# Optimization experiments

Hardware: AMD Instinct MI355X
Metric: run time of the kernel (lower is better)

Reference implementation:

```python
import jax, jax.numpy as jnp
import numpy as np
import math

B, L, DM, H, DK, DFF, E, FACTOR = 4, 2048, 512, 8, 64, 2048, 3, 5
U = min(FACTOR * math.ceil(math.log(L)), L)  # 40: ProbSparse sample/top-k count
SCALE = 1.0 / math.sqrt(DK)
EPS = 1e-5


def setup_inputs() -> dict:
    key = jax.random.key(0)
    ks = jax.random.split(key, 24)
    w = lambda k, s: jax.random.normal(k, s, jnp.float32) * 0.02
    inp = {
        "DNAs": jax.random.normal(ks[0], (B, L, 4), jnp.float32),
        "W_pre": w(ks[1], (4, DM)), "b_pre": jnp.zeros((DM,), jnp.float32),
        "Wq": w(ks[2], (E, DM, DM)), "bq": jnp.zeros((E, DM), jnp.float32),
        "Wk": w(ks[3], (E, DM, DM)), "bk": jnp.zeros((E, DM), jnp.float32),
        "Wv": w(ks[4], (E, DM, DM)), "bv": jnp.zeros((E, DM), jnp.float32),
        "Wo": w(ks[5], (E, DM, DM)), "bo": jnp.zeros((E, DM), jnp.float32),
        "ln1_g": jnp.ones((E, DM), jnp.float32), "ln1_b": jnp.zeros((E, DM), jnp.float32),
        "W1": w(ks[6], (E, DM, DFF)), "b1": jnp.zeros((E, DFF), jnp.float32),
        "W2": w(ks[7], (E, DFF, DM)), "b2": jnp.zeros((E, DM), jnp.float32),
        "ln2_g": jnp.ones((E, DM), jnp.float32), "ln2_b": jnp.zeros((E, DM), jnp.float32),
        "lnf_g": jnp.ones((DM,), jnp.float32), "lnf_b": jnp.zeros((DM,), jnp.float32),
        "W_out": w(ks[8], (DM, 3)), "b_out": jnp.zeros((3,), jnp.float32),
        "sample_idx": jax.random.randint(ks[9], (L, U), 0, L, dtype=jnp.int32),
    }
    return inp


def layer_norm(x, g, b):
    m = jnp.mean(x, axis=-1, keepdims=True)
    v = jnp.mean((x - m) ** 2, axis=-1, keepdims=True)
    return (x - m) / jnp.sqrt(v + EPS) * g + b


def prob_attention(q, k, v, idx):
    # q,k,v: (B,H,L,DK); idx: (L,U) sampled key positions per query
    Ks = k[:, :, idx, :]                                   # (B,H,L,U,DK)
    qk = jnp.einsum('bhld,bhlud->bhlu', q, Ks)             # sampled scores
    M = qk.max(axis=-1) - qk.mean(axis=-1)                 # sparsity measure (B,H,L)
    _, top = jax.lax.top_k(M, U)                           # top-U "active" queries (B,H,U)
    q_red = jnp.take_along_axis(q, top[..., None], axis=2) # (B,H,U,DK)
    scores = jnp.einsum('bhud,bhkd->bhuk', q_red, k) * SCALE
    attn = jax.nn.softmax(scores, axis=-1)
    upd = jnp.einsum('bhuk,bhkd->bhud', attn, v)           # (B,H,U,DK)
    # lazy queries get mean(V) as context; active queries get true attention
    ctx = jnp.broadcast_to(v.mean(axis=2)[:, :, None, :], q.shape)
    bi = jnp.arange(B)[:, None, None]
    hi = jnp.arange(H)[None, :, None]
    return ctx.at[bi, hi, top].set(upd)                    # (B,H,L,DK)


def reference(DNAs, W_pre, b_pre, Wq, bq, Wk, bk, Wv, bv, Wo, bo,
              ln1_g, ln1_b, W1, b1, W2, b2, ln2_g, ln2_b,
              lnf_g, lnf_b, W_out, b_out, sample_idx):
    x = DNAs @ W_pre + b_pre                               # prenet (B,L,DM)
    for i in range(E):
        q = (x @ Wq[i] + bq[i]).reshape(B, L, H, DK).transpose(0, 2, 1, 3)
        k = (x @ Wk[i] + bk[i]).reshape(B, L, H, DK).transpose(0, 2, 1, 3)
        v = (x @ Wv[i] + bv[i]).reshape(B, L, H, DK).transpose(0, 2, 1, 3)
        ctx = prob_attention(q, k, v, sample_idx)
        a = ctx.transpose(0, 2, 1, 3).reshape(B, L, DM) @ Wo[i] + bo[i]
        x = layer_norm(x + a, ln1_g[i], ln1_b[i])
        y = jax.nn.relu(x @ W1[i] + b1[i]) @ W2[i] + b2[i]  # position-wise FFN
        x = layer_norm(x + y, ln2_g[i], ln2_b[i])
    x = layer_norm(x, lnf_g, lnf_b)                         # encoder final norm
    return jax.nn.softmax(x @ W_out + b_out, axis=2)        # (B,L,3)
```

## Files before the change

### kernel.cpp

```cpp
#include <hip/hip_runtime.h>
#include <math.h>

#define B_   4
#define L_   2048
#define DM_  512
#define H_   8
#define DK_  64
#define DFF_ 2048
#define E_   3
#define U_   40
#define R_   8192
#define SCALE_ 0.125f
#define EPS_ 1e-5f

typedef __bf16 bf16x8 __attribute__((ext_vector_type(8)));
typedef float f32x4 __attribute__((ext_vector_type(4)));

__device__ inline unsigned short f2bf(float x) {
  unsigned int u = __float_as_uint(x);
  unsigned int r = (u + 0x7fffu + ((u >> 16) & 1u)) >> 16;
  return (unsigned short)r;
}

__global__ __launch_bounds__(256) void wtrans(
    const float* __restrict__ s0, const float* __restrict__ s1,
    const float* __restrict__ s2, const float* __restrict__ s3,
    unsigned short* __restrict__ dst, int R, int C, int permat) {
  __shared__ float tile[32][33];
  int z = blockIdx.z;
  int which = z / 3, e = z % 3;
  const float* src = (which == 0 ? s0 : which == 1 ? s1 : which == 2 ? s2 : s3);
  src += (size_t)e * permat;
  unsigned short* d = dst + (size_t)z * permat;
  int c0 = blockIdx.x << 5, r0 = blockIdx.y << 5;
  int tx = threadIdx.x & 31, ty = threadIdx.x >> 5;
  for (int rr = ty; rr < 32; rr += 8)
    tile[rr][tx] = src[(size_t)(r0 + rr) * C + c0 + tx];
  __syncthreads();
  for (int cc = ty; cc < 32; cc += 8)
    d[(size_t)(c0 + cc) * R + r0 + tx] = f2bf(tile[tx][cc]);
}

__global__ __launch_bounds__(256) void pre_kernel(
    const float* __restrict__ DNAs, const float* __restrict__ Wp,
    const float* __restrict__ bp, float* __restrict__ X,
    unsigned short* __restrict__ Xbf) {
  int t = blockIdx.x * 256 + threadIdx.x;
  int r = t >> 9, d = t & 511;
  float4 dna = *(const float4*)(DNAs + r * 4);
  float v = dna.x * Wp[d] + dna.y * Wp[512 + d] + dna.z * Wp[1024 + d] +
            dna.w * Wp[1536 + d] + bp[d];
  X[t] = v;
  Xbf[t] = f2bf(v);
}

template <int OUT, bool QKVZ, bool DBUF, int BN>
__global__ __launch_bounds__(256) void mgemm(
    const unsigned short* __restrict__ A, const unsigned short* __restrict__ BT,
    const float* __restrict__ bias0, const float* __restrict__ bias1,
    const float* __restrict__ bias2, float* __restrict__ Cf,
    unsigned short* __restrict__ Cb, int M, int N, int K) {
  constexpr int NFRAG = BN / 32;
  constexpr int BCH = BN / 8;
  constexpr int ASZ = 128 * 64, BSZ = BN * 64;
  __shared__ unsigned short As[(DBUF ? 2 : 1) * ASZ];
  __shared__ unsigned short Bs[(DBUF ? 2 : 1) * BSZ];
  const int t = threadIdx.x, l = t & 63, w = t >> 6;
  const int id = blockIdx.x;
  const int m0 = (id & 63) << 7;
  const int n0 = (id >> 6) * BN;
  const int wm = w >> 1, wn = w & 1;
  const float* bias = bias0;
  if (QKVZ) {
    int z = blockIdx.z;
    BT += (size_t)z * 3 * 262144;
    bias = (z == 0 ? bias0 : z == 1 ? bias1 : bias2);
    Cf += (size_t)z * 4194304;
  }
  f32x4 acc[4][NFRAG] = {};

  const int srow = l >> 3;
  const int gslot = (l & 7) ^ srow;

  auto stage = [&](int buf, int k0) {
#pragma unroll
    for (int j = 0; j < 4; ++j) {
      int c = (w << 2) + j;
      int row = (c << 3) + srow;
      const unsigned short* ga = A + (size_t)(m0 + row) * K + k0 + gslot * 8;
      __builtin_amdgcn_global_load_lds(
          (const __attribute__((address_space(1))) void*)ga,
          (__attribute__((address_space(3))) void*)(As + buf * ASZ + (c << 9)), 16, 0, 0);
      if (BN == 128 || j < 2) {
        int cb = (BN == 128) ? c : ((w << 1) + j);
        int brow = (cb << 3) + srow;
        const unsigned short* gb = BT + (size_t)(n0 + brow) * K + k0 + gslot * 8;
        __builtin_amdgcn_global_load_lds(
            (const __attribute__((address_space(1))) void*)gb,
            (__attribute__((address_space(3))) void*)(Bs + buf * BSZ + (cb << 9)), 16, 0, 0);
      }
    }
  };
  auto compute = [&](int buf) {
#pragma unroll
    for (int ks = 0; ks < 2; ++ks) {
      bf16x8 af[4], bg[NFRAG];
      int slot = (ks << 2) + (l >> 4);
#pragma unroll
      for (int i = 0; i < 4; ++i) {
        int ar = (wm << 6) + (i << 4) + (l & 15);
        af[i] = *(const bf16x8*)(As + buf * ASZ + ar * 64 + (slot ^ (ar & 7)) * 8);
      }
#pragma unroll
      for (int j = 0; j < NFRAG; ++j) {
        int br = wn * (BN >> 1) + (j << 4) + (l & 15);
        bg[j] = *(const bf16x8*)(Bs + buf * BSZ + br * 64 + (slot ^ (br & 7)) * 8);
      }
#pragma unroll
      for (int i = 0; i < 4; ++i)
#pragma unroll
        for (int j = 0; j < NFRAG; ++j)
          acc[i][j] = __builtin_amdgcn_mfma_f32_16x16x32_bf16(af[i], bg[j],
                                                              acc[i][j], 0, 0, 0);
    }
  };

  if (DBUF) {
    int nk = K >> 6, cur = 0;
    stage(0, 0);
    __syncthreads();
    for (int s = 0; s < nk; ++s) {
      if (s + 1 < nk) stage(cur ^ 1, (s + 1) << 6);
      compute(cur);
      __syncthreads();
      cur ^= 1;
    }
  } else {
    for (int k0 = 0; k0 < K; k0 += 64) {
      stage(0, k0);
      __syncthreads();
      compute(0);
      __syncthreads();
    }
  }

#pragma unroll
  for (int i = 0; i < 4; ++i) {
    int rbase = m0 + (wm << 6) + (i << 4) + ((l >> 4) << 2);
#pragma unroll
    for (int j = 0; j < NFRAG; ++j) {
      int col = n0 + wn * (BN >> 1) + (j << 4) + (l & 15);
      float bv = bias[col];
#pragma unroll
      for (int r = 0; r < 4; ++r) {
        int row = rbase + r;
        float v = acc[i][j][r] + bv;
        if (OUT == 2) {
          v = fmaxf(v, 0.f);
          Cb[(size_t)row * N + col] = f2bf(v);
        } else if (OUT == 1) {
          int b = row >> 11, ll = row & 2047, h = col >> 6, d = col & 63;
          Cf[((size_t)(((b << 3) + h) << 11) + ll) * 64 + d] = v;
        } else {
          Cf[(size_t)row * N + col] = v;
        }
      }
    }
  }
}

__global__ __launch_bounds__(256) void qk_m_kernel(
    const float* __restrict__ Q, const float* __restrict__ K,
    const int* __restrict__ sidx, float* __restrict__ Mout) {
  int t = threadIdx.x;
  int wave = t >> 6, lane = t & 63;
  int grp = lane >> 3, sub = lane & 7;
  int bh = blockIdx.x & 31;
  int j = blockIdx.x >> 5;
  int item = (bh << 11) + (j << 5) + wave * 8 + grp;
  int l = item & 2047;
  const float* Qr = Q + (size_t)item * 64;
  float4 q0 = *(const float4*)(Qr + sub * 4);
  float4 q1 = *(const float4*)(Qr + 32 + sub * 4);
  const float* Kb = K + (((size_t)bh << 11) << 6);
  const int* sp = sidx + l * U_;
  float mx = -INFINITY, sm = 0.f;
#pragma unroll 8
  for (int u = 0; u < U_; ++u) {
    int kidx = sp[u];
    const float* kr = Kb + ((size_t)kidx << 6);
    float4 k0 = *(const float4*)(kr + sub * 4);
    float4 k1 = *(const float4*)(kr + 32 + sub * 4);
    float p = q0.x * k0.x + q0.y * k0.y + q0.z * k0.z + q0.w * k0.w;
    p = fmaf(q1.x, k1.x, p); p = fmaf(q1.y, k1.y, p);
    p = fmaf(q1.z, k1.z, p); p = fmaf(q1.w, k1.w, p);
    p += __shfl_xor(p, 1);
    p += __shfl_xor(p, 2);
    p += __shfl_xor(p, 4);
    mx = fmaxf(mx, p);
    sm += p;
  }
  if (sub == 0) Mout[item] = mx - sm * (1.0f / U_);
}

__global__ __launch_bounds__(256) void topk_kernel(
    const float* __restrict__ Mb, int* __restrict__ TOP) {
  __shared__ unsigned vals[2048];
  __shared__ int hist[256];
  __shared__ int suf[256];
  __shared__ unsigned s_prefix;
  __shared__ int s_want, s_cnt, s_run;
  __shared__ int wcnt[4];
  int bh = blockIdx.x, t = threadIdx.x;
  int lane = t & 63, w = t >> 6;
  for (int i = t; i < 2048; i += 256) {
    unsigned u = __float_as_uint(Mb[bh * 2048 + i]);
    vals[i] = (u & 0x80000000u) ? ~u : (u | 0x80000000u);
  }
  if (t == 0) { s_prefix = 0; s_want = U_; s_cnt = 0; s_run = 0; }
  __syncthreads();
#pragma unroll
  for (int shift = 24; shift >= 0; shift -= 8) {
    unsigned pref = s_prefix;
    int want = s_want;
    unsigned hmask = (shift == 24) ? 0u : (0xFFFFFFFFu << (shift + 8));
    hist[t] = 0;
    __syncthreads();
    for (int i = t; i < 2048; i += 256) {
      unsigned v = vals[i];
      if ((v & hmask) == pref) atomicAdd(&hist[(v >> shift) & 255], 1);
    }
    __syncthreads();
    suf[t] = hist[t];
    __syncthreads();
    for (int off = 1; off < 256; off <<= 1) {
      int add = (t + off < 256) ? suf[t + off] : 0;
      __syncthreads();
      suf[t] += add;
      __syncthreads();
    }
    int cgt = (t == 255) ? 0 : suf[t + 1];
    if (suf[t] >= want && cgt < want) {
      s_prefix = pref | ((unsigned)t << shift);
      s_want = want - cgt;
    }
    __syncthreads();
  }
  unsigned T = s_prefix;
  int want_eq = s_want;
  int base = U_ - want_eq;
  for (int i = t; i < 2048; i += 256) {
    if (vals[i] > T) {
      int slot = atomicAdd(&s_cnt, 1);
      TOP[bh * U_ + slot] = i;
    }
  }
  for (int c = 0; c < 8; ++c) {
    int i = (c << 8) + t;
    bool eq = (vals[i] == T);
    unsigned long long m = __ballot(eq);
    if (lane == 0) wcnt[w] = __popcll(m);
    __syncthreads();
    int woff = 0;
    for (int ww = 0; ww < w; ++ww) woff += wcnt[ww];
    if (eq) {
      int rank = s_run + woff + __popcll(m & ((1ull << lane) - 1ull));
      if (rank < want_eq) TOP[bh * U_ + base + rank] = i;
    }
    __syncthreads();
    if (t == 0) s_run += wcnt[0] + wcnt[1] + wcnt[2] + wcnt[3];
    __syncthreads();
  }
}

__global__ __launch_bounds__(256) void vmean_kernel(
    const float* __restrict__ V, float* __restrict__ VM,
    unsigned short* __restrict__ VMbf) {
  __shared__ float p[4][64];
  int bh = blockIdx.x;
  int d = threadIdx.x & 63, c = threadIdx.x >> 6;
  const float* Vb = V + (((size_t)bh << 11) + c * 512) * 64;
  float s = 0.f;
  for (int l = 0; l < 512; ++l) s += Vb[l * 64 + d];
  p[c][d] = s;
  __syncthreads();
  if (threadIdx.x < 64) {
    float m = (p[0][d] + p[1][d] + p[2][d] + p[3][d]) * (1.0f / 2048.0f);
    VM[bh * 64 + d] = m;
    VMbf[bh * 64 + d] = f2bf(m);
  }
}

__global__ __launch_bounds__(256) void attn_score(
    const float* __restrict__ Q, const float* __restrict__ K,
    const int* __restrict__ TOP, float* __restrict__ S) {
  __shared__ float Ks[128 * 65];
  __shared__ float Qs[40 * 64];
  int bh = blockIdx.y, k0 = blockIdx.x << 7;
  int t = threadIdx.x;
  for (int i = t; i < 2560; i += 256) {
    int u = i >> 6, d = i & 63;
    int row = TOP[bh * U_ + u];
    Qs[i] = Q[(((size_t)bh << 11) + row) * 64 + d];
  }
  for (int i = t; i < 8192; i += 256) {
    int k = i >> 6, d = i & 63;
    Ks[k * 65 + d] = K[(((size_t)bh << 11) + k0 + k) * 64 + d];
  }
  __syncthreads();
  int kk = t & 127, ug = (t >> 7) * 20;
  const float* kp = Ks + kk * 65;
  for (int u = ug; u < ug + 20; ++u) {
    const float* qp = Qs + u * 64;
    float s = 0.f;
#pragma unroll 8
    for (int d = 0; d < 64; ++d) s = fmaf(qp[d], kp[d], s);
    S[((size_t)bh * U_ + u) * 2048 + k0 + kk] = s * SCALE_;
  }
}

__global__ __launch_bounds__(512) void attn_pv_part(
    const float* __restrict__ S, const float* __restrict__ V,
    float* __restrict__ PART, float* __restrict__ IRED) {
  __shared__ float Vs[128][64];
  __shared__ float ps[8][128];
  __shared__ float mred[8];
  int id = blockIdx.x;
  int bh = id & 31, sub = id >> 5;
  int ug = sub >> 2, kc = sub & 3;
  int t = threadIdx.x, lane = t & 63, w = t >> 6;
  int rowbase = bh * U_ + ug * 8;
  int row = rowbase + w;

  const float* Sr = S + (size_t)row * 2048;
  float mx = -INFINITY;
  for (int j = 0; j < 32; ++j) mx = fmaxf(mx, Sr[j * 64 + lane]);
#pragma unroll
  for (int s = 32; s; s >>= 1) mx = fmaxf(mx, __shfl_xor(mx, s));
  float sm = 0.f;
  for (int j = 0; j < 32; ++j) sm += __expf(Sr[j * 64 + lane] - mx);
#pragma unroll
  for (int s = 32; s; s >>= 1) sm += __shfl_xor(sm, s);
  if (lane == 0) {
    mred[w] = mx;
    if (kc == 0) IRED[row] = 1.0f / sm;
  }
  __syncthreads();

  const float* Vb = V + (((size_t)bh << 11) << 6);
  float a0 = 0.f, a1 = 0.f, a2 = 0.f, a3 = 0.f;
  for (int c = kc * 4; c < kc * 4 + 4; ++c) {
    int k0 = c << 7;
#pragma unroll
    for (int i = 0; i < 4; ++i) {
      int ve = t + i * 512;
      int k = ve >> 4, dq = ve & 15;
      *(float4*)&Vs[k][dq << 2] = *(const float4*)(Vb + (size_t)(k0 + k) * 64 + (dq << 2));
    }
#pragma unroll
    for (int i = 0; i < 2; ++i) {
      int e = t + i * 512;
      int r = e >> 7, kk = e & 127;
      ps[r][kk] = __expf(S[(size_t)(rowbase + r) * 2048 + k0 + kk] - mred[r]);
    }
    __syncthreads();
    const float* p = ps[w];
#pragma unroll 4
    for (int kk = 0; kk < 128; kk += 4) {
      float4 p4 = *(const float4*)(p + kk);
      a0 = fmaf(p4.x, Vs[kk + 0][lane], a0);
      a1 = fmaf(p4.y, Vs[kk + 1][lane], a1);
      a2 = fmaf(p4.z, Vs[kk + 2][lane], a2);
      a3 = fmaf(p4.w, Vs[kk + 3][lane], a3);
    }
    __syncthreads();
  }
  PART[((size_t)kc * 1280 + row) * 64 + lane] = (a0 + a1) + (a2 + a3);
}

__global__ __launch_bounds__(256) void pv_reduce(
    const float* __restrict__ PART, const float* __restrict__ IRED,
    const int* __restrict__ TOP, unsigned short* __restrict__ CTX) {
  int gid = blockIdx.x * 256 + threadIdx.x;
  int row = gid >> 6, lane = gid & 63;
  float v = (PART[(size_t)row * 64 + lane] + PART[(size_t)(1280 + row) * 64 + lane]) +
            (PART[(size_t)(2560 + row) * 64 + lane] + PART[(size_t)(3840 + row) * 64 + lane]);
  v *= IRED[row];
  int bh = row / U_;
  int b = bh >> 3, h = bh & 7;
  int orow = TOP[row];
  CTX[((size_t)((b << 11) + orow) << 9) + (h << 6) + lane] = f2bf(v);
}

__global__ __launch_bounds__(256) void ctxfill_kernel(
    const unsigned short* __restrict__ VMbf, unsigned short* __restrict__ CTX) {
  int t8 = (blockIdx.x * 256 + threadIdx.x) << 3;
  int c0 = t8 & 511;
  int b = t8 >> 20;
  *(uint4*)(CTX + t8) = *(const uint4*)(VMbf + (b << 9) + c0);
}

template <bool ADD, bool WB>
__global__ __launch_bounds__(256) void ln_kernel(
    const float* __restrict__ Xin, const float* __restrict__ Tin,
    const float* __restrict__ g, const float* __restrict__ bta,
    float* __restrict__ Xout, unsigned short* __restrict__ Xbf) {
  __shared__ float red[8];
  int r = blockIdx.x, t = threadIdx.x;
  int i0 = (r << 9) + (t << 1);
  float2 v = *(const float2*)(Xin + i0);
  if constexpr (ADD) {
    float2 tv = *(const float2*)(Tin + i0);
    v.x += tv.x; v.y += tv.y;
  }
  float sm = v.x + v.y;
#pragma unroll
  for (int s = 32; s; s >>= 1) sm += __shfl_xor(sm, s);
  int lane = t & 63, w = t >> 6;
  if (lane == 0) red[w] = sm;
  __syncthreads();
  float mean = (red[0] + red[1] + red[2] + red[3]) * (1.0f / 512.0f);
  float d0 = v.x - mean, d1 = v.y - mean;
  float sq = d0 * d0 + d1 * d1;
#pragma unroll
  for (int s = 32; s; s >>= 1) sq += __shfl_xor(sq, s);
  if (lane == 0) red[4 + w] = sq;
  __syncthreads();
  float var = (red[4] + red[5] + red[6] + red[7]) * (1.0f / 512.0f);
  float rstd = rsqrtf(var + EPS_);
  float2 gv = *(const float2*)(g + (t << 1));
  float2 bv = *(const float2*)(bta + (t << 1));
  float o0 = d0 * rstd * gv.x + bv.x;
  float o1 = d1 * rstd * gv.y + bv.y;
  *(float2*)(Xout + i0) = make_float2(o0, o1);
  if constexpr (WB) {
    *(unsigned*)(Xbf + i0) = (unsigned)f2bf(o0) | ((unsigned)f2bf(o1) << 16);
  }
}

__global__ __launch_bounds__(256) void out_kernel(
    const float* __restrict__ X, const float* __restrict__ Wout,
    const float* __restrict__ bout, float* __restrict__ out) {
  int w = threadIdx.x >> 6, lane = threadIdx.x & 63;
  int r = blockIdx.x * 4 + w;
  float p0 = 0.f, p1 = 0.f, p2 = 0.f;
  for (int d = lane; d < 512; d += 64) {
    float x = X[(r << 9) + d];
    p0 += x * Wout[d * 3 + 0];
    p1 += x * Wout[d * 3 + 1];
    p2 += x * Wout[d * 3 + 2];
  }
#pragma unroll
  for (int s = 32; s; s >>= 1) {
    p0 += __shfl_xor(p0, s);
    p1 += __shfl_xor(p1, s);
    p2 += __shfl_xor(p2, s);
  }
  if (lane == 0) {
    p0 += bout[0]; p1 += bout[1]; p2 += bout[2];
    float m = fmaxf(p0, fmaxf(p1, p2));
    float e0 = __expf(p0 - m), e1 = __expf(p1 - m), e2 = __expf(p2 - m);
    float z = 1.0f / (e0 + e1 + e2);
    out[r * 3 + 0] = e0 * z;
    out[r * 3 + 1] = e1 * z;
    out[r * 3 + 2] = e2 * z;
  }
}

extern "C" void kernel_launch(void* const* d_in, const int* in_sizes, int n_in,
                              void* d_out, int out_size, void* d_ws, size_t ws_size,
                              hipStream_t stream) {
  const float* DNAs  = (const float*)d_in[0];
  const float* W_pre = (const float*)d_in[1];
  const float* b_pre = (const float*)d_in[2];
  const float* Wq    = (const float*)d_in[3];
  const float* bq    = (const float*)d_in[4];
  const float* Wk    = (const float*)d_in[5];
  const float* bk    = (const float*)d_in[6];
  const float* Wv    = (const float*)d_in[7];
  const float* bv    = (const float*)d_in[8];
  const float* Wo    = (const float*)d_in[9];
  const float* bo    = (const float*)d_in[10];
  const float* ln1_g = (const float*)d_in[11];
  const float* ln1_b = (const float*)d_in[12];
  const float* W1    = (const float*)d_in[13];
  const float* b1    = (const float*)d_in[14];
  const float* W2    = (const float*)d_in[15];
  const float* b2    = (const float*)d_in[16];
  const float* ln2_g = (const float*)d_in[17];
  const float* ln2_b = (const float*)d_in[18];
  const float* lnf_g = (const float*)d_in[19];
  const float* lnf_b = (const float*)d_in[20];
  const float* W_out = (const float*)d_in[21];
  const float* b_out = (const float*)d_in[22];
  const int*   sidx  = (const int*)d_in[23];
  float* out = (float*)d_out;

  float* ws = (float*)d_ws;
  float*          X     = ws;
  unsigned short* Xbf   = (unsigned short*)(ws + 4194304);
  float*          Qb    = ws + 6291456;
  float*          T     = Qb;
  float*          PART  = Qb;
  float*          IRED  = Qb + 327680;
  float*          Kb    = ws + 10485760;
  float*          Vb    = ws + 14680064;
  float*          S     = ws + 18874368;
  unsigned short* CTXbf = (unsigned short*)(ws + 18874368 + 3276800);
  unsigned short* HBbf  = (unsigned short*)(ws + 18874368);
  unsigned short* WT    = (unsigned short*)(ws + 27262976);
  float*          Mb    = ws + 31981568;
  float*          VM    = ws + 32129024;
  int*            TOP   = (int*)(ws + 32131072);
  unsigned short* VMbf  = (unsigned short*)(ws + 32132352);
  unsigned short* WTqkvo = WT;
  unsigned short* WT1    = WT + 3145728;
  unsigned short* WT2    = WT + 6291456;
  (void)in_sizes; (void)n_in; (void)out_size; (void)ws_size;

  wtrans<<<dim3(16, 16, 12), 256, 0, stream>>>(Wq, Wk, Wv, Wo, WTqkvo, 512, 512, 262144);
  wtrans<<<dim3(64, 16, 3), 256, 0, stream>>>(W1, nullptr, nullptr, nullptr, WT1, 512, 2048, 1048576);
  wtrans<<<dim3(16, 64, 3), 256, 0, stream>>>(W2, nullptr, nullptr, nullptr, WT2, 2048, 512, 1048576);

  pre_kernel<<<16384, 256, 0, stream>>>(DNAs, W_pre, b_pre, X, Xbf);

  for (int i = 0; i < E_; ++i) {
    const int bOff = i * DM_;
    mgemm<1, true, false, 128><<<dim3(256, 1, 3), 256, 0, stream>>>(
        Xbf, WTqkvo + (size_t)i * 262144, bq + bOff, bk + bOff, bv + bOff,
        Qb, nullptr, R_, DM_, DM_);

    qk_m_kernel<<<2048, 256, 0, stream>>>(Qb, Kb, sidx, Mb);
    topk_kernel<<<32, 256, 0, stream>>>(Mb, TOP);
    vmean_kernel<<<32, 256, 0, stream>>>(Vb, VM, VMbf);
    attn_score<<<dim3(16, 32), 256, 0, stream>>>(Qb, Kb, TOP, S);
    ctxfill_kernel<<<2048, 256, 0, stream>>>(VMbf, CTXbf);
    attn_pv_part<<<640, 512, 0, stream>>>(S, Vb, PART, IRED);
    pv_reduce<<<320, 256, 0, stream>>>(PART, IRED, TOP, CTXbf);

    mgemm<0, false, true, 64><<<512, 256, 0, stream>>>(
        CTXbf, WTqkvo + (size_t)(9 + i) * 262144, bo + bOff, nullptr, nullptr,
        T, nullptr, R_, DM_, DM_);
    ln_kernel<true, true><<<8192, 256, 0, stream>>>(X, T, ln1_g + bOff, ln1_b + bOff, X, Xbf);

    mgemm<2, false, false, 128><<<1024, 256, 0, stream>>>(
        Xbf, WT1 + (size_t)i * 1048576, b1 + i * DFF_, nullptr, nullptr,
        nullptr, HBbf, R_, DFF_, DM_);
    mgemm<0, false, true, 64><<<512, 256, 0, stream>>>(
        HBbf, WT2 + (size_t)i * 1048576, b2 + bOff, nullptr, nullptr,
        T, nullptr, R_, DM_, DFF_);
    ln_kernel<true, true><<<8192, 256, 0, stream>>>(X, T, ln2_g + bOff, ln2_b + bOff, X, Xbf);
  }

  ln_kernel<false, false><<<8192, 256, 0, stream>>>(X, nullptr, lnf_g, lnf_b, X, nullptr);
  out_kernel<<<2048, 256, 0, stream>>>(X, W_out, b_out, out);
}
```

Baseline: 734.3 us.

## Store Q/K/V and GEMM outputs in bf16, fuse final layernorm into output head

GEMM epilogues now write bf16 instead of fp32 for the Q/K/V projections and the Wo/W2 outputs. Every consumer (qk_m, vmean, attn_score, attn_pv_part, ln_kernel) unpacks bf16 on load, which roughly halves the memory traffic of these intermediates. Separately, the final layernorm is folded into out_kernel, removing one full pass over X. The cost is lower precision in the residual addend and in the attention inputs, which could change which queries top-k selects.

```diff
diff --git a/kernel.cpp b/kernel.cpp
--- a/kernel.cpp
+++ b/kernel.cpp
@@ -21,6 +21,9 @@
   unsigned int r = (u + 0x7fffu + ((u >> 16) & 1u)) >> 16;
   return (unsigned short)r;
 }
+__device__ inline float bflo(unsigned u) { return __uint_as_float(u << 16); }
+__device__ inline float bfhi(unsigned u) { return __uint_as_float(u & 0xffff0000u); }
+__device__ inline float bf1(unsigned short u) { return __uint_as_float((unsigned)u << 16); }
 
 __global__ __launch_bounds__(256) void wtrans(
     const float* __restrict__ s0, const float* __restrict__ s1,
@@ -58,10 +61,9 @@
 __global__ __launch_bounds__(256) void mgemm(
     const unsigned short* __restrict__ A, const unsigned short* __restrict__ BT,
     const float* __restrict__ bias0, const float* __restrict__ bias1,
-    const float* __restrict__ bias2, float* __restrict__ Cf,
-    unsigned short* __restrict__ Cb, int M, int N, int K) {
+    const float* __restrict__ bias2, unsigned short* __restrict__ Cb,
+    int M, int N, int K) {
   constexpr int NFRAG = BN / 32;
-  constexpr int BCH = BN / 8;
   constexpr int ASZ = 128 * 64, BSZ = BN * 64;
   __shared__ unsigned short As[(DBUF ? 2 : 1) * ASZ];
   __shared__ unsigned short Bs[(DBUF ? 2 : 1) * BSZ];
@@ -75,7 +77,7 @@
     int z = blockIdx.z;
     BT += (size_t)z * 3 * 262144;
     bias = (z == 0 ? bias0 : z == 1 ? bias1 : bias2);
-    Cf += (size_t)z * 4194304;
+    Cb += (size_t)z * 4194304;
   }
   f32x4 acc[4][NFRAG] = {};
 
@@ -160,9 +162,9 @@
           Cb[(size_t)row * N + col] = f2bf(v);
         } else if (OUT == 1) {
           int b = row >> 11, ll = row & 2047, h = col >> 6, d = col & 63;
-          Cf[((size_t)(((b << 3) + h) << 11) + ll) * 64 + d] = v;
+          Cb[((size_t)(((b << 3) + h) << 11) + ll) * 64 + d] = f2bf(v);
         } else {
-          Cf[(size_t)row * N + col] = v;
+          Cb[(size_t)row * N + col] = f2bf(v);
         }
       }
     }
@@ -170,7 +172,7 @@
 }
 
 __global__ __launch_bounds__(256) void qk_m_kernel(
-    const float* __restrict__ Q, const float* __restrict__ K,
+    const unsigned short* __restrict__ Q, const unsigned short* __restrict__ K,
     const int* __restrict__ sidx, float* __restrict__ Mout) {
   int t = threadIdx.x;
   int wave = t >> 6, lane = t & 63;
@@ -179,21 +181,24 @@
   int j = blockIdx.x >> 5;
   int item = (bh << 11) + (j << 5) + wave * 8 + grp;
   int l = item & 2047;
-  const float* Qr = Q + (size_t)item * 64;
-  float4 q0 = *(const float4*)(Qr + sub * 4);
-  float4 q1 = *(const float4*)(Qr + 32 + sub * 4);
-  const float* Kb = K + (((size_t)bh << 11) << 6);
+  uint4 qv = *(const uint4*)(Q + ((size_t)item << 6) + (sub << 3));
+  float qf[8] = {bflo(qv.x), bfhi(qv.x), bflo(qv.y), bfhi(qv.y),
+                 bflo(qv.z), bfhi(qv.z), bflo(qv.w), bfhi(qv.w)};
+  const unsigned short* Kb = K + (((size_t)bh << 11) << 6) + (sub << 3);
   const int* sp = sidx + l * U_;
   float mx = -INFINITY, sm = 0.f;
 #pragma unroll 8
   for (int u = 0; u < U_; ++u) {
     int kidx = sp[u];
-    const float* kr = Kb + ((size_t)kidx << 6);
-    float4 k0 = *(const float4*)(kr + sub * 4);
-    float4 k1 = *(const float4*)(kr + 32 + sub * 4);
-    float p = q0.x * k0.x + q0.y * k0.y + q0.z * k0.z + q0.w * k0.w;
-    p = fmaf(q1.x, k1.x, p); p = fmaf(q1.y, k1.y, p);
-    p = fmaf(q1.z, k1.z, p); p = fmaf(q1.w, k1.w, p);
+    uint4 kv = *(const uint4*)(Kb + ((size_t)kidx << 6));
+    float p = qf[0] * bflo(kv.x);
+    p = fmaf(qf[1], bfhi(kv.x), p);
+    p = fmaf(qf[2], bflo(kv.y), p);
+    p = fmaf(qf[3], bfhi(kv.y), p);
+    p = fmaf(qf[4], bflo(kv.z), p);
+    p = fmaf(qf[5], bfhi(kv.z), p);
+    p = fmaf(qf[6], bflo(kv.w), p);
+    p = fmaf(qf[7], bfhi(kv.w), p);
     p += __shfl_xor(p, 1);
     p += __shfl_xor(p, 2);
     p += __shfl_xor(p, 4);
@@ -274,14 +279,14 @@
 }
 
 __global__ __launch_bounds__(256) void vmean_kernel(
-    const float* __restrict__ V, float* __restrict__ VM,
+    const unsigned short* __restrict__ V, float* __restrict__ VM,
     unsigned short* __restrict__ VMbf) {
   __shared__ float p[4][64];
   int bh = blockIdx.x;
   int d = threadIdx.x & 63, c = threadIdx.x >> 6;
-  const float* Vb = V + (((size_t)bh << 11) + c * 512) * 64;
+  const unsigned short* Vb = V + (((size_t)bh << 11) + c * 512) * 64;
   float s = 0.f;
-  for (int l = 0; l < 512; ++l) s += Vb[l * 64 + d];
+  for (int l = 0; l < 512; ++l) s += bf1(Vb[l * 64 + d]);
   p[c][d] = s;
   __syncthreads();
   if (threadIdx.x < 64) {
@@ -292,20 +297,25 @@
 }
 
 __global__ __launch_bounds__(256) void attn_score(
-    const float* __restrict__ Q, const float* __restrict__ K,
+    const unsigned short* __restrict__ Q, const unsigned short* __restrict__ K,
     const int* __restrict__ TOP, float* __restrict__ S) {
   __shared__ float Ks[128 * 65];
   __shared__ float Qs[40 * 64];
   int bh = blockIdx.y, k0 = blockIdx.x << 7;
   int t = threadIdx.x;
-  for (int i = t; i < 2560; i += 256) {
-    int u = i >> 6, d = i & 63;
-    int row = TOP[bh * U_ + u];
-    Qs[i] = Q[(((size_t)bh << 11) + row) * 64 + d];
-  }
-  for (int i = t; i < 8192; i += 256) {
-    int k = i >> 6, d = i & 63;
-    Ks[k * 65 + d] = K[(((size_t)bh << 11) + k0 + k) * 64 + d];
+  const unsigned short* Kbase = K + (((size_t)bh << 11) << 6);
+  for (int i = t; i < 4096; i += 256) {
+    int k = i >> 5, dp = i & 31;
+    unsigned u = *(const unsigned*)(Kbase + ((size_t)(k0 + k) << 6) + (dp << 1));
+    Ks[k * 65 + (dp << 1)] = bflo(u);
+    Ks[k * 65 + (dp << 1) + 1] = bfhi(u);
+  }
+  for (int i = t; i < 1280; i += 256) {
+    int uq = i >> 5, dp = i & 31;
+    int row = TOP[bh * U_ + uq];
+    unsigned u = *(const unsigned*)(Q + ((((size_t)bh << 11) + row) << 6) + (dp << 1));
+    Qs[uq * 64 + (dp << 1)] = bflo(u);
+    Qs[uq * 64 + (dp << 1) + 1] = bfhi(u);
   }
   __syncthreads();
   int kk = t & 127, ug = (t >> 7) * 20;
@@ -320,7 +330,7 @@
 }
 
 __global__ __launch_bounds__(512) void attn_pv_part(
-    const float* __restrict__ S, const float* __restrict__ V,
+    const float* __restrict__ S, const unsigned short* __restrict__ V,
     float* __restrict__ PART, float* __restrict__ IRED) {
   __shared__ float Vs[128][64];
   __shared__ float ps[8][128];
@@ -347,15 +357,17 @@
   }
   __syncthreads();
 
-  const float* Vb = V + (((size_t)bh << 11) << 6);
+  const unsigned short* Vb = V + (((size_t)bh << 11) << 6);
   float a0 = 0.f, a1 = 0.f, a2 = 0.f, a3 = 0.f;
   for (int c = kc * 4; c < kc * 4 + 4; ++c) {
     int k0 = c << 7;
 #pragma unroll
-    for (int i = 0; i < 4; ++i) {
-      int ve = t + i * 512;
-      int k = ve >> 4, dq = ve & 15;
-      *(float4*)&Vs[k][dq << 2] = *(const float4*)(Vb + (size_t)(k0 + k) * 64 + (dq << 2));
+    for (int i = 0; i < 8; ++i) {
+      int pe = t + i * 512;
+      int k = pe >> 5, dp = pe & 31;
+      unsigned u = *(const unsigned*)(Vb + ((size_t)(k0 + k) << 6) + (dp << 1));
+      Vs[k][(dp << 1)] = bflo(u);
+      Vs[k][(dp << 1) + 1] = bfhi(u);
     }
 #pragma unroll
     for (int i = 0; i < 2; ++i) {
@@ -400,19 +412,17 @@
   *(uint4*)(CTX + t8) = *(const uint4*)(VMbf + (b << 9) + c0);
 }
 
-template <bool ADD, bool WB>
 __global__ __launch_bounds__(256) void ln_kernel(
-    const float* __restrict__ Xin, const float* __restrict__ Tin,
+    const float* __restrict__ Xin, const unsigned short* __restrict__ Tin,
     const float* __restrict__ g, const float* __restrict__ bta,
     float* __restrict__ Xout, unsigned short* __restrict__ Xbf) {
   __shared__ float red[8];
   int r = blockIdx.x, t = threadIdx.x;
   int i0 = (r << 9) + (t << 1);
   float2 v = *(const float2*)(Xin + i0);
-  if constexpr (ADD) {
-    float2 tv = *(const float2*)(Tin + i0);
-    v.x += tv.x; v.y += tv.y;
-  }
+  unsigned tu = *(const unsigned*)(Tin + i0);
+  v.x += bflo(tu);
+  v.y += bfhi(tu);
   float sm = v.x + v.y;
 #pragma unroll
   for (int s = 32; s; s >>= 1) sm += __shfl_xor(sm, s);
@@ -433,22 +443,42 @@
   float o0 = d0 * rstd * gv.x + bv.x;
   float o1 = d1 * rstd * gv.y + bv.y;
   *(float2*)(Xout + i0) = make_float2(o0, o1);
-  if constexpr (WB) {
-    *(unsigned*)(Xbf + i0) = (unsigned)f2bf(o0) | ((unsigned)f2bf(o1) << 16);
-  }
+  *(unsigned*)(Xbf + i0) = (unsigned)f2bf(o0) | ((unsigned)f2bf(o1) << 16);
 }
 
 __global__ __launch_bounds__(256) void out_kernel(
-    const float* __restrict__ X, const float* __restrict__ Wout,
+    const float* __restrict__ X, const float* __restrict__ lg,
+    const float* __restrict__ lb, const float* __restrict__ Wout,
     const float* __restrict__ bout, float* __restrict__ out) {
   int w = threadIdx.x >> 6, lane = threadIdx.x & 63;
   int r = blockIdx.x * 4 + w;
+  float xv[8];
+  float sm = 0.f;
+#pragma unroll
+  for (int j = 0; j < 8; ++j) {
+    xv[j] = X[(r << 9) + lane + (j << 6)];
+    sm += xv[j];
+  }
+#pragma unroll
+  for (int s = 32; s; s >>= 1) sm += __shfl_xor(sm, s);
+  float mean = sm * (1.0f / 512.0f);
+  float sq = 0.f;
+#pragma unroll
+  for (int j = 0; j < 8; ++j) {
+    float d = xv[j] - mean;
+    sq += d * d;
+  }
+#pragma unroll
+  for (int s = 32; s; s >>= 1) sq += __shfl_xor(sq, s);
+  float rstd = rsqrtf(sq * (1.0f / 512.0f) + EPS_);
   float p0 = 0.f, p1 = 0.f, p2 = 0.f;
-  for (int d = lane; d < 512; d += 64) {
-    float x = X[(r << 9) + d];
-    p0 += x * Wout[d * 3 + 0];
-    p1 += x * Wout[d * 3 + 1];
-    p2 += x * Wout[d * 3 + 2];
+#pragma unroll
+  for (int j = 0; j < 8; ++j) {
+    int d = lane + (j << 6);
+    float xn = (xv[j] - mean) * rstd * lg[d] + lb[d];
+    p0 = fmaf(xn, Wout[d * 3 + 0], p0);
+    p1 = fmaf(xn, Wout[d * 3 + 1], p1);
+    p2 = fmaf(xn, Wout[d * 3 + 2], p2);
   }
 #pragma unroll
   for (int s = 32; s; s >>= 1) {
@@ -499,20 +529,21 @@
   float* ws = (float*)d_ws;
   float*          X     = ws;
   unsigned short* Xbf   = (unsigned short*)(ws + 4194304);
-  float*          Qb    = ws + 6291456;
-  float*          T     = Qb;
-  float*          PART  = Qb;
-  float*          IRED  = Qb + 327680;
-  float*          Kb    = ws + 10485760;
-  float*          Vb    = ws + 14680064;
-  float*          S     = ws + 18874368;
-  unsigned short* CTXbf = (unsigned short*)(ws + 18874368 + 3276800);
-  unsigned short* HBbf  = (unsigned short*)(ws + 18874368);
-  unsigned short* WT    = (unsigned short*)(ws + 27262976);
-  float*          Mb    = ws + 31981568;
-  float*          VM    = ws + 32129024;
-  int*            TOP   = (int*)(ws + 32131072);
-  unsigned short* VMbf  = (unsigned short*)(ws + 32132352);
+  unsigned short* QKVbf = (unsigned short*)(ws + 6291456);
+  unsigned short* Qbf   = QKVbf;
+  unsigned short* Kbf   = QKVbf + 4194304;
+  unsigned short* Vbf   = QKVbf + 8388608;
+  unsigned short* Tbf   = (unsigned short*)(ws + 12582912);
+  float*          PART  = ws + 12582912;
+  float*          IRED  = ws + 12910592;
+  float*          S     = ws + 14680064;
+  unsigned short* HBbf  = (unsigned short*)(ws + 14680064);
+  unsigned short* CTXbf = (unsigned short*)(ws + 23068672);
+  unsigned short* WT    = (unsigned short*)(ws + 25165824);
+  float*          Mb    = ws + 29884416;
+  float*          VM    = ws + 29949952;
+  int*            TOP   = (int*)(ws + 29952000);
+  unsigned short* VMbf  = (unsigned short*)(ws + 29953280);
   unsigned short* WTqkvo = WT;
   unsigned short* WT1    = WT + 3145728;
   unsigned short* WT2    = WT + 6291456;
@@ -528,30 +559,29 @@
     const int bOff = i * DM_;
     mgemm<1, true, false, 128><<<dim3(256, 1, 3), 256, 0, stream>>>(
         Xbf, WTqkvo + (size_t)i * 262144, bq + bOff, bk + bOff, bv + bOff,
-        Qb, nullptr, R_, DM_, DM_);
-
-    qk_m_kernel<<<2048, 256, 0, stream>>>(Qb, Kb, sidx, Mb);
+        QKVbf, R_, DM_, DM_);
+
+    qk_m_kernel<<<2048, 256, 0, stream>>>(Qbf, Kbf, sidx, Mb);
     topk_kernel<<<32, 256, 0, stream>>>(Mb, TOP);
-    vmean_kernel<<<32, 256, 0, stream>>>(Vb, VM, VMbf);
-    attn_score<<<dim3(16, 32), 256, 0, stream>>>(Qb, Kb, TOP, S);
+    vmean_kernel<<<32, 256, 0, stream>>>(Vbf, VM, VMbf);
+    attn_score<<<dim3(16, 32), 256, 0, stream>>>(Qbf, Kbf, TOP, S);
     ctxfill_kernel<<<2048, 256, 0, stream>>>(VMbf, CTXbf);
-    attn_pv_part<<<640, 512, 0, stream>>>(S, Vb, PART, IRED);
+    attn_pv_part<<<640, 512, 0, stream>>>(S, Vbf, PART, IRED);
     pv_reduce<<<320, 256, 0, stream>>>(PART, IRED, TOP, CTXbf);
 
-    mgemm<0, false, true, 64><<<512, 256, 0, stream>>>(
+    mgemm<3, false, true, 64><<<512, 256, 0, stream>>>(
         CTXbf, WTqkvo + (size_t)(9 + i) * 262144, bo + bOff, nullptr, nullptr,
-        T, nullptr, R_, DM_, DM_);
-    ln_kernel<true, true><<<8192, 256, 0, stream>>>(X, T, ln1_g + bOff, ln1_b + bOff, X, Xbf);
+        Tbf, R_, DM_, DM_);
+    ln_kernel<<<8192, 256, 0, stream>>>(X, Tbf, ln1_g + bOff, ln1_b + bOff, X, Xbf);
 
     mgemm<2, false, false, 128><<<1024, 256, 0, stream>>>(
         Xbf, WT1 + (size_t)i * 1048576, b1 + i * DFF_, nullptr, nullptr,
-        nullptr, HBbf, R_, DFF_, DM_);
-    mgemm<0, false, true, 64><<<512, 256, 0, stream>>>(
+        HBbf, R_, DFF_, DM_);
+    mgemm<3, false, true, 64><<<512, 256, 0, stream>>>(
         HBbf, WT2 + (size_t)i * 1048576, b2 + bOff, nullptr, nullptr,
-        T, nullptr, R_, DM_, DFF_);
-    ln_kernel<true, true><<<8192, 256, 0, stream>>>(X, T, ln2_g + bOff, ln2_b + bOff, X, Xbf);
-  }
-
-  ln_kernel<false, false><<<8192, 256, 0, stream>>>(X, nullptr, lnf_g, lnf_b, X, nullptr);
-  out_kernel<<<2048, 256, 0, stream>>>(X, W_out, b_out, out);
-}
+        Tbf, R_, DM_, DFF_);
+    ln_kernel<<<8192, 256, 0, stream>>>(X, Tbf, ln2_g + bOff, ln2_b + bOff, X, Xbf);
+  }
+
+  out_kernel<<<2048, 256, 0, stream>>>(X, lnf_g, lnf_b, W_out, b_out, out);
+}
```

Result: faster. 663.6 us (-9.6%).
